# Performance work log

Measured on AMD Instinct MI355X. Metric: run time of the kernel, lower is better.

Reference implementation:

```python
import jax, jax.numpy as jnp
import numpy as np

# --- constants matching ElectrostaticEnergy defaults ---
KE = 14.399645351950548
KEHALF = KE / 2.0
CUTON = 2.5
CUTOFF = 7.5
LR_CUTOFF = 10.0
CUTON16 = CUTON ** 16
CUT_RCONSTANT = LR_CUTOFF ** 15 / (LR_CUTOFF ** 16 + CUTON ** 16) ** (17.0 / 16.0)
CUT_CONSTANT = 1.0 / (CUTON ** 16 + LR_CUTOFF ** 16) ** (1.0 / 16.0) + LR_CUTOFF ** 16 / (LR_CUTOFF ** 16 + CUTON ** 16) ** (17.0 / 16.0)

N_ATOMS = 102400   # total atoms
N_PAIRS = N_ATOMS * 64  # 6,553,600 edges
N_MOL = 2048       # molecules (atoms per molecule = 50)


def switch_function(x):
    """SpookyNet-style smooth switch: 1 below cuton, 0 above cutoff."""
    t = (CUTOFF - x) / (CUTOFF - CUTON)

    def comp(u):
        u_safe = jnp.where(u <= 0, jnp.ones_like(u), u)
        return jnp.where(u <= 0, jnp.zeros_like(u), jnp.exp(-1.0 / u_safe))

    fp = comp(t)
    fm = comp(1.0 - t)
    return jnp.where(t <= 0, jnp.zeros_like(t),
                     jnp.where(t >= 1, jnp.ones_like(t), fp / (fp + fm)))


def setup_inputs() -> dict:
    key = jax.random.key(0)
    k1, k2, k3, k4, k5 = jax.random.split(key, 5)
    atomic_numbers = jax.random.randint(k1, (N_ATOMS,), 1, 10, dtype=jnp.int32)
    q = 0.1 * jax.random.normal(k2, (N_ATOMS,), dtype=jnp.float32)  # partial charges
    # uniform components in [0.8, 6.5] -> d_ij roughly in [1.4, 11.2], spans all cutoffs
    r_ij = jax.random.uniform(k3, (N_PAIRS, 3), dtype=jnp.float32, minval=0.8, maxval=6.5)
    idx_i = jax.random.randint(k4, (N_PAIRS,), 0, N_ATOMS, dtype=jnp.int32)
    idx_j = jax.random.randint(k5, (N_PAIRS,), 0, N_ATOMS, dtype=jnp.int32)
    idx_m = jnp.repeat(jnp.arange(N_MOL, dtype=jnp.int32), N_ATOMS // N_MOL)  # sorted atom->mol map
    return {"atomic_numbers": atomic_numbers, "q": q, "r_ij": r_ij,
            "idx_i": idx_i, "idx_j": idx_j, "idx_m": idx_m, "maxm": N_MOL}


def reference(atomic_numbers, q, r_ij, idx_i, idx_j, idx_m, maxm):
    N = q.shape[0]
    d_ij = jnp.linalg.norm(r_ij, axis=1)                      # [P]
    fac = KEHALF * q[idx_i] * q[idx_j]                        # [P] gather
    f = switch_function(d_ij)                                 # [P]
    # lr_cutoff branch of the original module
    x_coulomb = 1.0 / d_ij + d_ij / (LR_CUTOFF ** 2) - 2.0 / LR_CUTOFF
    coulomb = jnp.where(d_ij < LR_CUTOFF, x_coulomb, jnp.zeros_like(d_ij))
    damped = (d_ij ** 16 + CUTON16) ** (-1.0 / 16.0) + (1.0 - f) * CUT_RCONSTANT * d_ij - CUT_CONSTANT
    e_edge = fac * (f * damped + (1.0 - f) * coulomb)         # [P]
    y_atom = jax.ops.segment_sum(e_edge, idx_i, num_segments=N)        # edge -> atom
    y = jax.ops.segment_sum(y_atom, idx_m, num_segments=maxm)          # atom -> molecule
    return y  # [maxm]
```

## Files before the change

### kernel.cpp

```cpp
#include <hip/hip_runtime.h>
#include <math.h>

#define NMOL   2048
#define APM    50u
#define BLOCK  512
#define GRID   2048
#define NREP   4

typedef float __attribute__((ext_vector_type(4))) fx4;
typedef int   __attribute__((ext_vector_type(4))) ix4;

#define KEHALF_F   7.199822675975274f
#define CUTON16_F  2328306.4365386963f
#define CUT_RCONST 0.01f
#define CUT_CONST  0.2f

__global__ void zero_rep_kernel(float* __restrict__ rep) {
    int i = blockIdx.x * blockDim.x + threadIdx.x;
    if (i < NREP * NMOL) rep[i] = 0.0f;
}

__device__ __forceinline__ float edge_energy(float x, float yv, float z,
                                             float qi, float qj) {
    const float d   = sqrtf(fmaf(x, x, fmaf(yv, yv, z * z)));
    const float fac = KEHALF_F * qi * qj;

    const float t  = fminf(fmaxf((7.5f - d) * 0.2f, 0.0f), 1.0f);
    const float fp = __expf(-__builtin_amdgcn_rcpf(t));
    const float fm = __expf(-__builtin_amdgcn_rcpf(1.0f - t));
    const float f  = fp * __builtin_amdgcn_rcpf(fp + fm);

    const float invd = __builtin_amdgcn_rcpf(d);
    const float coul = (d < 10.0f) ? fmaf(d, 0.01f, invd - 0.2f) : 0.0f;

    const float d2 = d * d, d4 = d2 * d2, d8 = d4 * d4, d16 = d8 * d8;
    const float damped = __expf(-0.0625f * __logf(d16 + CUTON16_F))
                       + (1.0f - f) * (CUT_RCONST * d) - CUT_CONST;

    return fac * (f * damped + (1.0f - f) * coul);
}

__launch_bounds__(BLOCK, 6)
__global__ void edge_energy_kernel(const float* __restrict__ q,
                                   const float* __restrict__ r,
                                   const int*   __restrict__ idx_i,
                                   const int*   __restrict__ idx_j,
                                   float*       __restrict__ rep,
                                   int P)
{
    __shared__ float bins[NMOL];
    for (int b = threadIdx.x; b < NMOL; b += BLOCK) bins[b] = 0.0f;
    __syncthreads();

    const int ngroups = P >> 2;
    const int GB      = GRID * BLOCK;
    const fx4* r4  = (const fx4*)r;
    const ix4* i4p = (const ix4*)idx_i;
    const ix4* j4p = (const ix4*)idx_j;

    for (int g = blockIdx.x * BLOCK + threadIdx.x; g < ngroups; g += 2 * GB) {
        const int  g2r  = g + GB;
        const bool has2 = g2r < ngroups;
        const int  g2   = has2 ? g2r : g;

        const fx4 ra1 = __builtin_nontemporal_load(&r4[3 * g  + 0]);
        const fx4 rb1 = __builtin_nontemporal_load(&r4[3 * g  + 1]);
        const fx4 rc1 = __builtin_nontemporal_load(&r4[3 * g  + 2]);
        const ix4 ii1 = __builtin_nontemporal_load(&i4p[g]);
        const ix4 jj1 = __builtin_nontemporal_load(&j4p[g]);
        const fx4 ra2 = __builtin_nontemporal_load(&r4[3 * g2 + 0]);
        const fx4 rb2 = __builtin_nontemporal_load(&r4[3 * g2 + 1]);
        const fx4 rc2 = __builtin_nontemporal_load(&r4[3 * g2 + 2]);
        const ix4 ii2 = __builtin_nontemporal_load(&i4p[g2]);
        const ix4 jj2 = __builtin_nontemporal_load(&j4p[g2]);

        const float qi10 = q[ii1.x], qj10 = q[jj1.x];
        const float qi11 = q[ii1.y], qj11 = q[jj1.y];
        const float qi12 = q[ii1.z], qj12 = q[jj1.z];
        const float qi13 = q[ii1.w], qj13 = q[jj1.w];
        const float qi20 = q[ii2.x], qj20 = q[jj2.x];
        const float qi21 = q[ii2.y], qj21 = q[jj2.y];
        const float qi22 = q[ii2.z], qj22 = q[jj2.z];
        const float qi23 = q[ii2.w], qj23 = q[jj2.w];

        const float e10 = edge_energy(ra1.x, ra1.y, ra1.z, qi10, qj10);
        const float e11 = edge_energy(ra1.w, rb1.x, rb1.y, qi11, qj11);
        const float e12 = edge_energy(rb1.z, rb1.w, rc1.x, qi12, qj12);
        const float e13 = edge_energy(rc1.y, rc1.z, rc1.w, qi13, qj13);

        atomicAdd(&bins[(unsigned)ii1.x / APM], e10);
        atomicAdd(&bins[(unsigned)ii1.y / APM], e11);
        atomicAdd(&bins[(unsigned)ii1.z / APM], e12);
        atomicAdd(&bins[(unsigned)ii1.w / APM], e13);

        const float e20 = edge_energy(ra2.x, ra2.y, ra2.z, qi20, qj20);
        const float e21 = edge_energy(ra2.w, rb2.x, rb2.y, qi21, qj21);
        const float e22 = edge_energy(rb2.z, rb2.w, rc2.x, qi22, qj22);
        const float e23 = edge_energy(rc2.y, rc2.z, rc2.w, qi23, qj23);

        if (has2) {
            atomicAdd(&bins[(unsigned)ii2.x / APM], e20);
            atomicAdd(&bins[(unsigned)ii2.y / APM], e21);
            atomicAdd(&bins[(unsigned)ii2.z / APM], e22);
            atomicAdd(&bins[(unsigned)ii2.w / APM], e23);
        }
    }

    for (int p = ((P >> 2) << 2) + blockIdx.x * BLOCK + threadIdx.x; p < P;
         p += GB) {
        const float e = edge_energy(r[3 * p], r[3 * p + 1], r[3 * p + 2],
                                    q[idx_i[p]], q[idx_j[p]]);
        atomicAdd(&bins[(unsigned)idx_i[p] / APM], e);
    }

    __syncthreads();
    float* yr = rep + (size_t)(blockIdx.x & (NREP - 1)) * NMOL;
    const int off = ((blockIdx.x >> 2) * 97) & (NMOL - 1);
    for (int b0 = threadIdx.x; b0 < NMOL; b0 += BLOCK) {
        const int b = (b0 + off) & (NMOL - 1);
        unsafeAtomicAdd(&yr[b], bins[b]);
    }
}

__global__ void final_kernel(const float* __restrict__ rep,
                             float*       __restrict__ y) {
    const int b = blockIdx.x * blockDim.x + threadIdx.x;
    if (b < NMOL) {
        float v = 0.0f;
        #pragma unroll
        for (int k = 0; k < NREP; ++k) v += rep[k * NMOL + b];
        y[b] = v;
    }
}

extern "C" void kernel_launch(void* const* d_in, const int* in_sizes, int n_in,
                              void* d_out, int out_size, void* d_ws, size_t ws_size,
                              hipStream_t stream) {
    const float* q     = (const float*)d_in[1];
    const float* r_ij  = (const float*)d_in[2];
    const int*   idx_i = (const int*)d_in[3];
    const int*   idx_j = (const int*)d_in[4];
    float*       y     = (float*)d_out;
    float*       rep   = (float*)d_ws;
    const int P = in_sizes[3];

    zero_rep_kernel<<<(NREP * NMOL + 255) / 256, 256, 0, stream>>>(rep);
    edge_energy_kernel<<<GRID, BLOCK, 0, stream>>>(q, r_ij, idx_i, idx_j, rep, P);
    final_kernel<<<(NMOL + 255) / 256, 256, 0, stream>>>(rep, y);
}
```

Before: 212.8 us.

## Stage fp16 charges in LDS to serve gathers, with larger blocks

A prep kernel converts charges to fp16. Each block of 1024 threads (grid 512) copies the first 73728 half-precision charges into LDS alongside the molecule bins, so most random q gathers become LDS reads. Indices beyond that range fall back to global fp16 loads. This cuts global gather traffic, but the per-block LDS fill adds work, occupancy is limited by the roughly 155KB of shared memory per block, and fp16 charges lose precision.

```diff
diff --git a/kernel.cpp b/kernel.cpp
--- a/kernel.cpp
+++ b/kernel.cpp
@@ -1,11 +1,15 @@
 #include <hip/hip_runtime.h>
+#include <hip/hip_fp16.h>
 #include <math.h>
 
 #define NMOL   2048
 #define APM    50u
-#define BLOCK  512
-#define GRID   2048
+#define NATOMS 102400
+#define BLOCK  1024
+#define GRID   512
 #define NREP   4
+#define NLDS   73728
+#define SMEM_BYTES (NMOL * 4 + NLDS * 2)
 
 typedef float __attribute__((ext_vector_type(4))) fx4;
 typedef int   __attribute__((ext_vector_type(4))) ix4;
@@ -15,8 +19,11 @@
 #define CUT_RCONST 0.01f
 #define CUT_CONST  0.2f
 
-__global__ void zero_rep_kernel(float* __restrict__ rep) {
-    int i = blockIdx.x * blockDim.x + threadIdx.x;
+__global__ void prep_kernel(const float* __restrict__ q,
+                            __half* __restrict__ qh,
+                            float* __restrict__ rep) {
+    const int i = blockIdx.x * blockDim.x + threadIdx.x;
+    if (i < NATOMS) qh[i] = __float2half_rn(q[i]);
     if (i < NREP * NMOL) rep[i] = 0.0f;
 }
 
@@ -40,16 +47,24 @@
     return fac * (f * damped + (1.0f - f) * coul);
 }
 
-__launch_bounds__(BLOCK, 6)
-__global__ void edge_energy_kernel(const float* __restrict__ q,
-                                   const float* __restrict__ r,
-                                   const int*   __restrict__ idx_i,
-                                   const int*   __restrict__ idx_j,
-                                   float*       __restrict__ rep,
+__launch_bounds__(BLOCK, 4)
+__global__ void edge_energy_kernel(const __half* __restrict__ qh,
+                                   const float*  __restrict__ r,
+                                   const int*    __restrict__ idx_i,
+                                   const int*    __restrict__ idx_j,
+                                   float*        __restrict__ rep,
                                    int P)
 {
-    __shared__ float bins[NMOL];
+    extern __shared__ char smem[];
+    float*  bins   = (float*)smem;
+    __half* q_lds  = (__half*)(smem + NMOL * 4);
+
     for (int b = threadIdx.x; b < NMOL; b += BLOCK) bins[b] = 0.0f;
+    {
+        const uint4* src = (const uint4*)qh;
+        uint4*       dst = (uint4*)q_lds;
+        for (int t = threadIdx.x; t < NLDS / 8; t += BLOCK) dst[t] = src[t];
+    }
     __syncthreads();
 
     const int ngroups = P >> 2;
@@ -57,6 +72,8 @@
     const fx4* r4  = (const fx4*)r;
     const ix4* i4p = (const ix4*)idx_i;
     const ix4* j4p = (const ix4*)idx_j;
+
+    #define GETQ(j) ((j) < NLDS ? __half2float(q_lds[j]) : __half2float(qh[j]))
 
     for (int g = blockIdx.x * BLOCK + threadIdx.x; g < ngroups; g += 2 * GB) {
         const int  g2r  = g + GB;
@@ -74,14 +91,14 @@
         const ix4 ii2 = __builtin_nontemporal_load(&i4p[g2]);
         const ix4 jj2 = __builtin_nontemporal_load(&j4p[g2]);
 
-        const float qi10 = q[ii1.x], qj10 = q[jj1.x];
-        const float qi11 = q[ii1.y], qj11 = q[jj1.y];
-        const float qi12 = q[ii1.z], qj12 = q[jj1.z];
-        const float qi13 = q[ii1.w], qj13 = q[jj1.w];
-        const float qi20 = q[ii2.x], qj20 = q[jj2.x];
-        const float qi21 = q[ii2.y], qj21 = q[jj2.y];
-        const float qi22 = q[ii2.z], qj22 = q[jj2.z];
-        const float qi23 = q[ii2.w], qj23 = q[jj2.w];
+        const float qi10 = GETQ(ii1.x), qj10 = GETQ(jj1.x);
+        const float qi11 = GETQ(ii1.y), qj11 = GETQ(jj1.y);
+        const float qi12 = GETQ(ii1.z), qj12 = GETQ(jj1.z);
+        const float qi13 = GETQ(ii1.w), qj13 = GETQ(jj1.w);
+        const float qi20 = GETQ(ii2.x), qj20 = GETQ(jj2.x);
+        const float qi21 = GETQ(ii2.y), qj21 = GETQ(jj2.y);
+        const float qi22 = GETQ(ii2.z), qj22 = GETQ(jj2.z);
+        const float qi23 = GETQ(ii2.w), qj23 = GETQ(jj2.w);
 
         const float e10 = edge_energy(ra1.x, ra1.y, ra1.z, qi10, qj10);
         const float e11 = edge_energy(ra1.w, rb1.x, rb1.y, qi11, qj11);
@@ -109,9 +126,10 @@
     for (int p = ((P >> 2) << 2) + blockIdx.x * BLOCK + threadIdx.x; p < P;
          p += GB) {
         const float e = edge_energy(r[3 * p], r[3 * p + 1], r[3 * p + 2],
-                                    q[idx_i[p]], q[idx_j[p]]);
+                                    GETQ(idx_i[p]), GETQ(idx_j[p]));
         atomicAdd(&bins[(unsigned)idx_i[p] / APM], e);
     }
+    #undef GETQ
 
     __syncthreads();
     float* yr = rep + (size_t)(blockIdx.x & (NREP - 1)) * NMOL;
@@ -141,10 +159,13 @@
     const int*   idx_i = (const int*)d_in[3];
     const int*   idx_j = (const int*)d_in[4];
     float*       y     = (float*)d_out;
-    float*       rep   = (float*)d_ws;
     const int P = in_sizes[3];
 
-    zero_rep_kernel<<<(NREP * NMOL + 255) / 256, 256, 0, stream>>>(rep);
-    edge_energy_kernel<<<GRID, BLOCK, 0, stream>>>(q, r_ij, idx_i, idx_j, rep, P);
+    __half* qh  = (__half*)d_ws;
+    float*  rep = (float*)((char*)d_ws + (size_t)NATOMS * 2);
+
+    prep_kernel<<<(NATOMS + 255) / 256, 256, 0, stream>>>(q, qh, rep);
+    edge_energy_kernel<<<GRID, BLOCK, SMEM_BYTES, stream>>>(qh, r_ij, idx_i,
+                                                            idx_j, rep, P);
     final_kernel<<<(NMOL + 255) / 256, 256, 0, stream>>>(rep, y);
 }
```

After: 204.8 us. 3.8% less time.
